# Kernel tuning notes

Hardware: AMD Instinct MI355X
Metric: run time of the kernel (lower is better)

Reference implementation:

```python
import jax, jax.numpy as jnp
import numpy as np

DIM = 4096
N_HEADS = 32
N_KV_HEADS = 8
HEAD_DIM = DIM // N_HEADS  # 128
N_REP = N_HEADS // N_KV_HEADS  # 4
B, S = 1, 2048
ROPE_THETA = 500000.0


def setup_inputs() -> dict:
    key = jax.random.key(0)
    ks = jax.random.split(key, 5)
    sc = 0.02
    x = jax.random.normal(ks[0], (B, S, DIM), jnp.float32)
    wq = jax.random.normal(ks[1], (DIM, N_HEADS * HEAD_DIM), jnp.float32) * sc
    wk = jax.random.normal(ks[2], (DIM, N_KV_HEADS * HEAD_DIM), jnp.float32) * sc
    wv = jax.random.normal(ks[3], (DIM, N_KV_HEADS * HEAD_DIM), jnp.float32) * sc
    wo = jax.random.normal(ks[4], (N_HEADS * HEAD_DIM, DIM), jnp.float32) * sc
    # rotary frequencies: freqs_cis = exp(i * t * theta^(-2j/d)), j in [0, head_dim/2)
    inv_freq = 1.0 / (ROPE_THETA ** (jnp.arange(0, HEAD_DIM, 2, dtype=jnp.float32) / HEAD_DIM))
    t = jnp.arange(S, dtype=jnp.float32)
    ang = jnp.outer(t, inv_freq)  # (S, head_dim/2)
    freqs_cos = jnp.cos(ang)
    freqs_sin = jnp.sin(ang)
    # additive causal mask, broadcastable to (B, H, S, S)
    mask = jnp.where(jnp.triu(jnp.ones((S, S), bool), k=1), -jnp.inf, 0.0).astype(jnp.float32)[None, None]
    return {"x": x, "wq": wq, "wk": wk, "wv": wv, "wo": wo,
            "freqs_cos": freqs_cos, "freqs_sin": freqs_sin, "mask": mask}


def _apply_rotary(t, cos, sin):
    # t: (B, S, n, hd); complex multiply on consecutive pairs (x0,x1),(x2,x3),...
    b, s, n, hd = t.shape
    tr = t.reshape(b, s, n, hd // 2, 2)
    re, im = tr[..., 0], tr[..., 1]
    c = cos[None, :, None, :]
    sn = sin[None, :, None, :]
    out_re = re * c - im * sn
    out_im = re * sn + im * c
    return jnp.stack([out_re, out_im], axis=-1).reshape(b, s, n, hd)


def reference(x, wq, wk, wv, wo, freqs_cos, freqs_sin, mask):
    b, s, _ = x.shape
    xq = (x @ wq).reshape(b, s, N_HEADS, HEAD_DIM)
    xk = (x @ wk).reshape(b, s, N_KV_HEADS, HEAD_DIM)
    xv = (x @ wv).reshape(b, s, N_KV_HEADS, HEAD_DIM)
    xq = _apply_rotary(xq, freqs_cos, freqs_sin)
    xk = _apply_rotary(xk, freqs_cos, freqs_sin)
    # repeat_kv (GQA): expand kv heads to match query heads
    keys = jnp.repeat(xk, N_REP, axis=2)    # (b, s, H, hd)
    values = jnp.repeat(xv, N_REP, axis=2)
    # (b, H, s, hd)
    q = xq.transpose(0, 2, 1, 3)
    k = keys.transpose(0, 2, 1, 3)
    v = values.transpose(0, 2, 1, 3)
    scores = jnp.einsum('bhqd,bhkd->bhqk', q, k) / np.sqrt(HEAD_DIM).astype(np.float32)
    scores = scores + mask
    probs = jax.nn.softmax(scores.astype(jnp.float32), axis=-1).astype(q.dtype)
    out = jnp.einsum('bhqk,bhkd->bhqd', probs, v)
    out = out.transpose(0, 2, 1, 3).reshape(b, s, N_HEADS * HEAD_DIM)
    return out @ wo
```

## Files before the change

### kernel.cpp

```cpp
#include <hip/hip_runtime.h>
#include <cstdint>
#include <cstddef>

typedef _Float16 f16_t;
typedef f16_t f16x8 __attribute__((ext_vector_type(8)));
typedef float  floatx4 __attribute__((ext_vector_type(4)));

#define S_LEN 2048
#define DIM_  4096
#define NH    32
#define NKV   8
#define HD    128
#define KV_DIM (NKV * HD)
#define QLD   (DIM_ + 2 * KV_DIM)

__device__ __forceinline__ float bf16r(float x) {
    uint32_t u = __float_as_uint(x);
    u = (u + 0x7fffu + ((u >> 16) & 1u)) & 0xffff0000u;
    return __uint_as_float(u);
}

__device__ __forceinline__ void gload_lds16(const f16_t* g, f16_t* l) {
    __builtin_amdgcn_global_load_lds(
        (const __attribute__((address_space(1))) void*)g,
        (__attribute__((address_space(3))) void*)l, 16, 0, 0);
}

__global__ void f32_to_f16_kernel(const float* __restrict__ in,
                                  f16_t* __restrict__ out, int n) {
    int i = (blockIdx.x * blockDim.x + threadIdx.x) * 8;
    if (i >= n) return;
    float4 a = *(const float4*)(in + i);
    float4 b = *(const float4*)(in + i + 4);
    f16x8 o;
    o[0] = (f16_t)bf16r(a.x); o[1] = (f16_t)bf16r(a.y);
    o[2] = (f16_t)bf16r(a.z); o[3] = (f16_t)bf16r(a.w);
    o[4] = (f16_t)bf16r(b.x); o[5] = (f16_t)bf16r(b.y);
    o[6] = (f16_t)bf16r(b.z); o[7] = (f16_t)bf16r(b.w);
    *(f16x8*)(out + i) = o;
}

__global__ void transpose_weights_kernel(const float* __restrict__ wq,
                                         const float* __restrict__ wk,
                                         const float* __restrict__ wv,
                                         const float* __restrict__ wo,
                                         f16_t* __restrict__ wqkvT,
                                         f16_t* __restrict__ woT) {
    __shared__ float tile[32][33];
    int bid = blockIdx.x;
    const float* in; f16_t* out; int C;
    if (bid < 16384)      { in = wq; out = wqkvT;                          C = 4096; }
    else if (bid < 20480) { bid -= 16384; in = wk; out = wqkvT + (size_t)4096 * 4096; C = 1024; }
    else if (bid < 24576) { bid -= 20480; in = wv; out = wqkvT + (size_t)5120 * 4096; C = 1024; }
    else                  { bid -= 24576; in = wo; out = woT;              C = 4096; }
    int gpr = C / 32;
    int bx = (bid % gpr) * 32;
    int by = (bid / gpr) * 32;
    int tx = threadIdx.x, ty = threadIdx.y;
#pragma unroll
    for (int i = 0; i < 4; i++) {
        int r = ty + i * 8;
        tile[r][tx] = in[(size_t)(by + r) * C + bx + tx];
    }
    __syncthreads();
#pragma unroll
    for (int i = 0; i < 4; i++) {
        int r = ty + i * 8;
        out[(size_t)(bx + r) * 4096 + by + tx] = (f16_t)bf16r(tile[tx][r]);
    }
}

__global__ void transpose_f16_kernel(const f16_t* __restrict__ in,
                                     f16_t* __restrict__ out,
                                     int ldi, int ldo) {
    __shared__ float tile[32][33];
    int bx = blockIdx.x * 32;
    int by = blockIdx.y * 32;
    int tx = threadIdx.x, ty = threadIdx.y;
#pragma unroll
    for (int i = 0; i < 4; i++) {
        int r = ty + i * 8;
        tile[r][tx] = (float)in[(size_t)(by + r) * ldi + bx + tx];
    }
    __syncthreads();
#pragma unroll
    for (int i = 0; i < 4; i++) {
        int r = ty + i * 8;
        out[(size_t)(bx + r) * ldo + by + tx] = (f16_t)tile[tx][r];
    }
}

__global__ void rope_qk_kernel(f16_t* __restrict__ QKV,
                               const float* __restrict__ fcos,
                               const float* __restrict__ fsin) {
    int c8 = (blockIdx.x * blockDim.x + threadIdx.x) * 8;
    int row = blockIdx.y;
    f16_t* p = QKV + (size_t)row * QLD + c8;
    f16x8 v = *(f16x8*)p;
    const float* cr = fcos + row * 64 + ((c8 & 127) >> 1);
    const float* sr = fsin + row * 64 + ((c8 & 127) >> 1);
    const float sc = (c8 < DIM_) ? 0.08838834764831845f : 1.0f;
#pragma unroll
    for (int u = 0; u < 4; u++) {
        float cc = bf16r(cr[u]), ss = bf16r(sr[u]);
        float re = (float)v[2 * u], im = (float)v[2 * u + 1];
        v[2 * u]     = (f16_t)((re * cc - im * ss) * sc);
        v[2 * u + 1] = (f16_t)((re * ss + im * cc) * sc);
    }
    *(f16x8*)p = v;
}

template <int BM, int BN, typename OutT>
__global__ __launch_bounds__(512, 2) void gemm_8p_kernel(
        const f16_t* __restrict__ A, const f16_t* __restrict__ BT,
        OutT* __restrict__ C, int M, int N, int K, int nbx) {
    constexpr int BK = 64;
    constexpr int MT = BM / 32;
    constexpr int NT = BN / 64;
    constexpr int MH = MT / 2;
    constexpr int AHALF = (BM / 2) * 64;
    constexpr int BHALF = (BN / 2) * 64;
    constexpr int BUF   = (BM + BN) * 64;
    constexpr int AJ = BM / 128;
    constexpr int BJ = BN / 128;

    __shared__ f16_t lds[2 * BUF];

    const int tid  = threadIdx.x;
    const int lane = tid & 63;
    const int wave = tid >> 6;
    const int quad = lane >> 4;
    const int l16  = lane & 15;
    const int wmi  = wave >> 2;
    const int wni  = wave & 3;

    const int nwg = gridDim.x;
    const int swz = (blockIdx.x & 7) * (nwg >> 3) + (blockIdx.x >> 3);
    const int m0 = (swz / nbx) * BM;
    const int n0 = (swz % nbx) * BN;

    const f16_t* srcA[2][AJ]; int dA[2][AJ];
    const f16_t* srcB[2][BJ]; int dB[2][BJ];
#pragma unroll
    for (int h = 0; h < 2; h++)
#pragma unroll
        for (int j = 0; j < AJ; j++) {
            int L = j * 8192 + tid * 16;
            int r = L >> 7;
            int c = ((L & 127) ^ (((L >> 9) & 1) << 5)) >> 1;
            srcA[h][j] = A + (size_t)(m0 + h * (BM / 2) + r) * K + c;
            dA[h][j] = h * AHALF + (L >> 1);
        }
#pragma unroll
    for (int h = 0; h < 2; h++)
#pragma unroll
        for (int j = 0; j < BJ; j++) {
            int L = j * 8192 + tid * 16;
            int r = L >> 7;
            int c = ((L & 127) ^ (((L >> 9) & 1) << 5)) >> 1;
            srcB[h][j] = BT + (size_t)(n0 + h * (BN / 2) + r) * K + c;
            dB[h][j] = 2 * AHALF + h * BHALF + (L >> 1);
        }

    auto stage_all = [&](int tt) {
        f16_t* base = lds + (tt & 1) * BUF;
        const int k0 = tt * BK;
#pragma unroll
        for (int h = 0; h < 2; h++)
#pragma unroll
            for (int j = 0; j < AJ; j++)
                gload_lds16(srcA[h][j] + k0, base + dA[h][j]);
#pragma unroll
        for (int h = 0; h < 2; h++)
#pragma unroll
            for (int j = 0; j < BJ; j++)
                gload_lds16(srcB[h][j] + k0, base + dB[h][j]);
    };

    floatx4 acc[MT][NT] = {};
    const int ntk = K / BK;

    stage_all(0);
    asm volatile("s_waitcnt vmcnt(0)" ::: "memory");
    __builtin_amdgcn_s_barrier();
    __builtin_amdgcn_sched_barrier(0);

#define PHASE(mh, ks, STAGE, DRAIN)                                           \
    {                                                                         \
        STAGE                                                                 \
        _Pragma("unroll")                                                     \
        for (int i = 0; i < MH; i++) {                                        \
            int r_ = ((mh) * MH + i) * 16 + l16;                              \
            int cb_ = (((ks) * 64) + quad * 16) ^ (((r_ >> 2) & 1) << 5);     \
            af[i] = *(const f16x8*)(Ab + r_ * 64 + (cb_ >> 1));               \
        }                                                                     \
        if ((mh) == 0) {                                                      \
            _Pragma("unroll")                                                 \
            for (int nt = 0; nt < NT; nt++) {                                 \
                int rb_ = (wni & 1) * 64 + nt * 16 + l16;                     \
                int cb_ = (((ks) * 64) + quad * 16) ^ (((rb_ >> 2) & 1) << 5);\
                bf[nt] = *(const f16x8*)(Bb + rb_ * 64 + (cb_ >> 1));         \
            }                                                                 \
        }                                                                     \
        __builtin_amdgcn_sched_barrier(0);                                    \
        __builtin_amdgcn_s_barrier();                                         \
        asm volatile("s_waitcnt lgkmcnt(0)" ::: "memory");                    \
        __builtin_amdgcn_sched_barrier(0);                                    \
        __builtin_amdgcn_s_setprio(1);                                        \
        _Pragma("unroll")                                                     \
        for (int i = 0; i < MH; i++)                                          \
            _Pragma("unroll")                                                 \
            for (int nt = 0; nt < NT; nt++)                                   \
                acc[(mh) * MH + i][nt] =                                      \
                    __builtin_amdgcn_mfma_f32_16x16x32_f16(                   \
                        af[i], bf[nt], acc[(mh) * MH + i][nt], 0, 0, 0);      \
        __builtin_amdgcn_s_setprio(0);                                        \
        DRAIN                                                                 \
        __builtin_amdgcn_sched_barrier(0);                                    \
        __builtin_amdgcn_s_barrier();                                         \
        __builtin_amdgcn_sched_barrier(0);                                    \
    }

    for (int t = 0; t < ntk; ++t) {
        const f16_t* Ab = lds + (t & 1) * BUF + wmi * AHALF;
        const f16_t* Bb = lds + (t & 1) * BUF + 2 * AHALF + (wni >> 1) * BHALF;
        const bool pre = (t + 1 < ntk);
        f16x8 af[MH], bf[NT];

        PHASE(0, 0, if (pre) stage_all(t + 1);, )
        PHASE(1, 0, , )
        PHASE(0, 1, , )
        PHASE(1, 1, ,
              if (pre) { asm volatile("s_waitcnt vmcnt(0)" ::: "memory"); })
    }
#undef PHASE

#pragma unroll
    for (int mt = 0; mt < MT; mt++)
#pragma unroll
        for (int nt = 0; nt < NT; nt++)
#pragma unroll
            for (int rg = 0; rg < 4; rg++) {
                int row = m0 + wmi * (BM / 2) + mt * 16 + quad * 4 + rg;
                int col = n0 + wni * 64 + nt * 16 + l16;
                C[(size_t)row * N + col] = (OutT)acc[mt][nt][rg];
            }
}

__global__ __launch_bounds__(512) void attn_kernel(
        const f16_t* __restrict__ QKV, const f16_t* __restrict__ Vt,
        f16_t* __restrict__ O) {
    constexpr int BK = 64;
    __shared__ f16_t Ks[BK * HD];
    __shared__ f16_t Vs[HD * BK];
    __shared__ f16_t Ps[8][16][72];

    const int tid  = threadIdx.x;
    const int lane = tid & 63;
    const int wave = tid >> 6;
    const int quad = lane >> 4;
    const int l16  = lane & 15;

    const int bid = blockIdx.x;
    const int h   = bid & 31;
    const int g   = bid >> 5;
    const int qt  = (g < 8) ? g : 23 - g;
    const int q0  = qt * 128;
    const int hkv = h >> 2;

    const int qrow = q0 + wave * 16 + l16;
    const f16_t* Qg = QKV + (size_t)qrow * QLD + h * HD;
    f16x8 qf[4];
#pragma unroll
    for (int c = 0; c < 4; c++) qf[c] = *(const f16x8*)(Qg + c * 32 + quad * 8);

    floatx4 o_acc[8] = {};
    floatx4 l_acc = {0.f, 0.f, 0.f, 0.f};
    float m_run[4];
#pragma unroll
    for (int i = 0; i < 4; i++) m_run[i] = -1e30f;

    f16x8 ones;
#pragma unroll
    for (int i = 0; i < 8; i++) ones[i] = (f16_t)1.0f;

    const int q_lo = q0 + wave * 16;
    const int q_hi = q_lo + 15;
    const int ntiles = q0 / BK + 2;

    const int rK = tid >> 4;
    const int cK = (((tid & 15) * 16) ^ ((rK & 7) << 4)) >> 1;
    const f16_t* pK = QKV + (size_t)rK * QLD + DIM_ + hkv * HD + cK;
    const int rV = tid >> 3;
    const int cV = (((tid & 7) * 16) ^ ((rV & 7) << 4)) >> 1;
    const f16_t* pV = Vt + (size_t)hkv * HD * S_LEN + (size_t)rV * S_LEN + cV;
    f16_t* KsD0 = Ks + tid * 8;  f16_t* KsD1 = KsD0 + 4096;
    f16_t* VsD0 = Vs + tid * 8;  f16_t* VsD1 = VsD0 + 4096;

    for (int t = 0; t < ntiles; t++) {
        const int k0 = t * BK;

        gload_lds16(pK + (size_t)k0 * QLD, KsD0);
        gload_lds16(pK + (size_t)(k0 + 32) * QLD, KsD1);
        gload_lds16(pV + k0, VsD0);
        gload_lds16(pV + k0 + (size_t)64 * S_LEN, VsD1);
        asm volatile("s_waitcnt vmcnt(0)" ::: "memory");
        __syncthreads();

        if (k0 <= q_hi) {
            floatx4 sc4[4] = {};
#pragma unroll
            for (int nt = 0; nt < 4; nt++) {
                const int r = nt * 16 + l16;
#pragma unroll
                for (int ks = 0; ks < 4; ks++) {
                    int cb = (ks * 64 + quad * 16) ^ ((r & 7) << 4);
                    f16x8 kf = *(const f16x8*)(Ks + r * 128 + (cb >> 1));
                    sc4[nt] = __builtin_amdgcn_mfma_f32_16x16x32_f16(qf[ks], kf, sc4[nt], 0, 0, 0);
                }
            }

            if ((k0 + BK - 1) > q_lo) {
#pragma unroll
                for (int nt = 0; nt < 4; nt++)
#pragma unroll
                    for (int rg = 0; rg < 4; rg++) {
                        int qg = q_lo + quad * 4 + rg;
                        int kg = k0 + nt * 16 + l16;
                        if (kg > qg) sc4[nt][rg] = -1e30f;
                    }
            }

            float m_t[4];
#pragma unroll
            for (int rg = 0; rg < 4; rg++) {
                float m = fmaxf(fmaxf(sc4[0][rg], sc4[1][rg]), fmaxf(sc4[2][rg], sc4[3][rg]));
#pragma unroll
                for (int off = 8; off >= 1; off >>= 1)
                    m = fmaxf(m, __shfl_xor(m, off, 64));
                m_t[rg] = m;
            }
            int grow = (m_t[0] > m_run[0] + 8.f) | (m_t[1] > m_run[1] + 8.f) |
                       (m_t[2] > m_run[2] + 8.f) | (m_t[3] > m_run[3] + 8.f);
            if (__any(grow)) {
                float alpha[4];
#pragma unroll
                for (int rg = 0; rg < 4; rg++) {
                    float mn = fmaxf(m_run[rg], m_t[rg]);
                    alpha[rg] = __expf(m_run[rg] - mn);
                    m_run[rg] = mn;
                }
#pragma unroll
                for (int dt = 0; dt < 8; dt++)
#pragma unroll
                    for (int rg = 0; rg < 4; rg++) o_acc[dt][rg] *= alpha[rg];
#pragma unroll
                for (int rg = 0; rg < 4; rg++) l_acc[rg] *= alpha[rg];
            }

#pragma unroll
            for (int nt = 0; nt < 4; nt++)
#pragma unroll
                for (int rg = 0; rg < 4; rg++)
                    Ps[wave][quad * 4 + rg][nt * 16 + l16] =
                        (f16_t)__expf(sc4[nt][rg] - m_run[rg]);
            asm volatile("s_waitcnt lgkmcnt(0)" ::: "memory");
            __builtin_amdgcn_sched_barrier(0);

#pragma unroll
            for (int ks = 0; ks < 2; ks++) {
                f16x8 pf = *(const f16x8*)&Ps[wave][l16][ks * 32 + quad * 8];
                l_acc = __builtin_amdgcn_mfma_f32_16x16x32_f16(pf, ones, l_acc, 0, 0, 0);
#pragma unroll
                for (int dt = 0; dt < 8; dt++) {
                    const int r = dt * 16 + l16;
                    int cb = (ks * 64 + quad * 16) ^ ((r & 7) << 4);
                    f16x8 vf = *(const f16x8*)(Vs + r * 64 + (cb >> 1));
                    o_acc[dt] = __builtin_amdgcn_mfma_f32_16x16x32_f16(pf, vf, o_acc[dt], 0, 0, 0);
                }
            }
        }
        __syncthreads();
    }

#pragma unroll
    for (int rg = 0; rg < 4; rg++) {
        float inv_l = 1.0f / l_acc[rg];
#pragma unroll
        for (int dt = 0; dt < 8; dt++) {
            int row = q0 + wave * 16 + quad * 4 + rg;
            int col = h * HD + dt * 16 + l16;
            O[(size_t)row * (NH * HD) + col] = (f16_t)(o_acc[dt][rg] * inv_l);
        }
    }
}

extern "C" void kernel_launch(void* const* d_in, const int* in_sizes, int n_in,
                              void* d_out, int out_size, void* d_ws, size_t ws_size,
                              hipStream_t stream) {
    const float* x    = (const float*)d_in[0];
    const float* wq   = (const float*)d_in[1];
    const float* wk   = (const float*)d_in[2];
    const float* wv   = (const float*)d_in[3];
    const float* wo   = (const float*)d_in[4];
    const float* fcos = (const float*)d_in[5];
    const float* fsin = (const float*)d_in[6];
    float* out = (float*)d_out;

    char* ws = (char*)d_ws;
    constexpr size_t MB = 1024 * 1024;
    f16_t* xb    = (f16_t*)(ws + 0 * MB);
    f16_t* wqkvT = (f16_t*)(ws + 16 * MB);
    f16_t* woT   = (f16_t*)(ws + 64 * MB);
    f16_t* QKVb  = (f16_t*)(ws + 96 * MB);
    f16_t* Vt    = (f16_t*)(ws + 120 * MB);
    f16_t* attnb = (f16_t*)(ws + 124 * MB);

    f32_to_f16_kernel<<<S_LEN * DIM_ / 8 / 256, 256, 0, stream>>>(x, xb, S_LEN * DIM_);
    transpose_weights_kernel<<<40960, dim3(32, 8), 0, stream>>>(wq, wk, wv, wo, wqkvT, woT);

    gemm_8p_kernel<256, 256, f16_t><<<192, 512, 0, stream>>>(
        xb, wqkvT, QKVb, S_LEN, QLD, DIM_, QLD / 256);

    rope_qk_kernel<<<dim3(5, S_LEN), 128, 0, stream>>>(QKVb, fcos, fsin);
    transpose_f16_kernel<<<dim3(KV_DIM / 32, S_LEN / 32), dim3(32, 8), 0, stream>>>(
        QKVb + 5120, Vt, QLD, S_LEN);

    attn_kernel<<<512, 512, 0, stream>>>(QKVb, Vt, attnb);

    gemm_8p_kernel<128, 256, float><<<256, 512, 0, stream>>>(
        attnb, woT, out, S_LEN, DIM_, DIM_, DIM_ / 256);
}
```

Baseline: 529.6 us.

## Restructure GEMM staging with row-XOR swizzle and one barrier per phase

Rewrites the GEMM main loop: the LDS swizzle changes from a coarse half-tile XOR to a per-row (r&7) 16-byte XOR, global-to-LDS addresses are computed inline instead of precomputed pointer arrays, and each phase uses a single barrier instead of two, waiting on lgkm/vm counters only in the last phase. The aim is fewer LDS bank conflicts, fewer live registers and less barrier overhead. NT is now fixed at 4, which is only correct when BN equals 256, and dropping the per-phase lgkmcnt wait relies on the compiler inserting waits before the MFMAs that use the loaded fragments.

```diff
diff --git a/kernel.cpp b/kernel.cpp
--- a/kernel.cpp
+++ b/kernel.cpp
@@ -116,13 +116,13 @@
         OutT* __restrict__ C, int M, int N, int K, int nbx) {
     constexpr int BK = 64;
     constexpr int MT = BM / 32;
-    constexpr int NT = BN / 64;
     constexpr int MH = MT / 2;
-    constexpr int AHALF = (BM / 2) * 64;
-    constexpr int BHALF = (BN / 2) * 64;
-    constexpr int BUF   = (BM + BN) * 64;
-    constexpr int AJ = BM / 128;
-    constexpr int BJ = BN / 128;
+    constexpr int NT = 4;
+    constexpr int AEL = BM * BK;
+    constexpr int BEL = BN * BK;
+    constexpr int BUF = AEL + BEL;
+    constexpr int AJ = AEL * 2 / 8192;
+    constexpr int BJ = BEL * 2 / 8192;
 
     __shared__ f16_t lds[2 * BUF];
 
@@ -139,42 +139,23 @@
     const int m0 = (swz / nbx) * BM;
     const int n0 = (swz % nbx) * BN;
 
-    const f16_t* srcA[2][AJ]; int dA[2][AJ];
-    const f16_t* srcB[2][BJ]; int dB[2][BJ];
-#pragma unroll
-    for (int h = 0; h < 2; h++)
+    auto stage_all = [&](int tt) {
+        f16_t* base = lds + (tt & 1) * BUF;
+        const int k0 = tt * BK;
 #pragma unroll
         for (int j = 0; j < AJ; j++) {
             int L = j * 8192 + tid * 16;
             int r = L >> 7;
-            int c = ((L & 127) ^ (((L >> 9) & 1) << 5)) >> 1;
-            srcA[h][j] = A + (size_t)(m0 + h * (BM / 2) + r) * K + c;
-            dA[h][j] = h * AHALF + (L >> 1);
+            int c = ((L & 127) ^ ((r & 7) << 4)) >> 1;
+            gload_lds16(A + (size_t)(m0 + r) * K + k0 + c, base + (L >> 1));
         }
-#pragma unroll
-    for (int h = 0; h < 2; h++)
 #pragma unroll
         for (int j = 0; j < BJ; j++) {
             int L = j * 8192 + tid * 16;
             int r = L >> 7;
-            int c = ((L & 127) ^ (((L >> 9) & 1) << 5)) >> 1;
-            srcB[h][j] = BT + (size_t)(n0 + h * (BN / 2) + r) * K + c;
-            dB[h][j] = 2 * AHALF + h * BHALF + (L >> 1);
+            int c = ((L & 127) ^ ((r & 7) << 4)) >> 1;
+            gload_lds16(BT + (size_t)(n0 + r) * K + k0 + c, base + AEL + (L >> 1));
         }
-
-    auto stage_all = [&](int tt) {
-        f16_t* base = lds + (tt & 1) * BUF;
-        const int k0 = tt * BK;
-#pragma unroll
-        for (int h = 0; h < 2; h++)
-#pragma unroll
-            for (int j = 0; j < AJ; j++)
-                gload_lds16(srcA[h][j] + k0, base + dA[h][j]);
-#pragma unroll
-        for (int h = 0; h < 2; h++)
-#pragma unroll
-            for (int j = 0; j < BJ; j++)
-                gload_lds16(srcB[h][j] + k0, base + dB[h][j]);
     };
 
     floatx4 acc[MT][NT] = {};
@@ -185,53 +166,51 @@
     __builtin_amdgcn_s_barrier();
     __builtin_amdgcn_sched_barrier(0);
 
-#define PHASE(mh, ks, STAGE, DRAIN)                                           \
-    {                                                                         \
-        STAGE                                                                 \
-        _Pragma("unroll")                                                     \
-        for (int i = 0; i < MH; i++) {                                        \
-            int r_ = ((mh) * MH + i) * 16 + l16;                              \
-            int cb_ = (((ks) * 64) + quad * 16) ^ (((r_ >> 2) & 1) << 5);     \
-            af[i] = *(const f16x8*)(Ab + r_ * 64 + (cb_ >> 1));               \
-        }                                                                     \
-        if ((mh) == 0) {                                                      \
-            _Pragma("unroll")                                                 \
-            for (int nt = 0; nt < NT; nt++) {                                 \
-                int rb_ = (wni & 1) * 64 + nt * 16 + l16;                     \
-                int cb_ = (((ks) * 64) + quad * 16) ^ (((rb_ >> 2) & 1) << 5);\
-                bf[nt] = *(const f16x8*)(Bb + rb_ * 64 + (cb_ >> 1));         \
-            }                                                                 \
-        }                                                                     \
-        __builtin_amdgcn_sched_barrier(0);                                    \
-        __builtin_amdgcn_s_barrier();                                         \
-        asm volatile("s_waitcnt lgkmcnt(0)" ::: "memory");                    \
-        __builtin_amdgcn_sched_barrier(0);                                    \
-        __builtin_amdgcn_s_setprio(1);                                        \
-        _Pragma("unroll")                                                     \
-        for (int i = 0; i < MH; i++)                                          \
-            _Pragma("unroll")                                                 \
-            for (int nt = 0; nt < NT; nt++)                                   \
-                acc[(mh) * MH + i][nt] =                                      \
-                    __builtin_amdgcn_mfma_f32_16x16x32_f16(                   \
-                        af[i], bf[nt], acc[(mh) * MH + i][nt], 0, 0, 0);      \
-        __builtin_amdgcn_s_setprio(0);                                        \
-        DRAIN                                                                 \
-        __builtin_amdgcn_sched_barrier(0);                                    \
-        __builtin_amdgcn_s_barrier();                                         \
-        __builtin_amdgcn_sched_barrier(0);                                    \
+#define PHASE(mh, ks, PRESTAGE, LASTP)                                         \
+    {                                                                          \
+        _Pragma("unroll")                                                      \
+        for (int i = 0; i < MH; i++) {                                         \
+            int r_ = ((mh) * MH + i) * 16 + l16;                               \
+            int cb_ = ((ks) * 64 + quad * 16) ^ ((r_ & 7) << 4);               \
+            af[i] = *(const f16x8*)(Ab + r_ * 64 + (cb_ >> 1));                \
+        }                                                                      \
+        if ((mh) == 0) {                                                       \
+            _Pragma("unroll")                                                  \
+            for (int nt = 0; nt < NT; nt++) {                                  \
+                int rb_ = (wni & 1) * 64 + nt * 16 + l16;                      \
+                int cb_ = ((ks) * 64 + quad * 16) ^ ((rb_ & 7) << 4);          \
+                bf[nt] = *(const f16x8*)(Bb + rb_ * 64 + (cb_ >> 1));          \
+            }                                                                  \
+        }                                                                      \
+        PRESTAGE                                                               \
+        if (LASTP) {                                                           \
+            asm volatile("s_waitcnt lgkmcnt(0)" ::: "memory");                 \
+            asm volatile("s_waitcnt vmcnt(0)" ::: "memory");                   \
+        }                                                                      \
+        __builtin_amdgcn_sched_barrier(0);                                     \
+        __builtin_amdgcn_s_barrier();                                          \
+        __builtin_amdgcn_sched_barrier(0);                                     \
+        __builtin_amdgcn_s_setprio(1);                                         \
+        _Pragma("unroll")                                                      \
+        for (int i = 0; i < MH; i++)                                           \
+            _Pragma("unroll")                                                  \
+            for (int nt = 0; nt < NT; nt++)                                    \
+                acc[(mh) * MH + i][nt] =                                       \
+                    __builtin_amdgcn_mfma_f32_16x16x32_f16(                    \
+                        af[i], bf[nt], acc[(mh) * MH + i][nt], 0, 0, 0);       \
+        __builtin_amdgcn_s_setprio(0);                                         \
     }
 
     for (int t = 0; t < ntk; ++t) {
-        const f16_t* Ab = lds + (t & 1) * BUF + wmi * AHALF;
-        const f16_t* Bb = lds + (t & 1) * BUF + 2 * AHALF + (wni >> 1) * BHALF;
+        const f16_t* Ab = lds + (t & 1) * BUF + wmi * (AEL / 2);
+        const f16_t* Bb = lds + (t & 1) * BUF + AEL + (wni >> 1) * (BEL / 2);
         const bool pre = (t + 1 < ntk);
         f16x8 af[MH], bf[NT];
 
-        PHASE(0, 0, if (pre) stage_all(t + 1);, )
-        PHASE(1, 0, , )
-        PHASE(0, 1, , )
-        PHASE(1, 1, ,
-              if (pre) { asm volatile("s_waitcnt vmcnt(0)" ::: "memory"); })
+        PHASE(0, 0, if (pre) stage_all(t + 1);, false)
+        PHASE(1, 0, , false)
+        PHASE(0, 1, , false)
+        PHASE(1, 1, , true)
     }
 #undef PHASE
 
```

Result: faster. 518.3 us (-2.1%).
